# Kernel optimization log

Hardware: AMD Instinct MI355X
Metric: run time of the kernel (lower is better)

## Reference

```python
import jax, jax.numpy as jnp
import numpy as np

HIDDEN = 2048
INTER = 4096
NUM_EXPERTS = 8
TOP_K = 4
BATCH, SEQ = 2, 2048
TOKENS = BATCH * SEQ


def setup_inputs() -> dict:
    key = jax.random.key(0)
    k_x, k_rw, k_tw, k_te, k_gu, k_dn = jax.random.split(key, 6)
    x = jax.random.normal(k_x, (BATCH, SEQ, HIDDEN), dtype=jnp.float32)
    # full router weights (passed through but unused by this patched forward)
    weights = jax.random.uniform(k_rw, (TOKENS, NUM_EXPERTS), dtype=jnp.float32)
    tw = jax.random.uniform(k_tw, (TOKENS, TOP_K), dtype=jnp.float32)
    top_weights = tw / jnp.sum(tw, axis=-1, keepdims=True)  # softmax-like, renormalize=False downstream
    top_experts = jax.random.randint(k_te, (TOKENS, TOP_K), 0, NUM_EXPERTS, dtype=jnp.int64)
    scale_gu = 1.0 / np.sqrt(HIDDEN)
    scale_dn = 1.0 / np.sqrt(INTER)
    gate_up_weights = jax.random.normal(k_gu, (NUM_EXPERTS, 2 * INTER, HIDDEN), dtype=jnp.float32) * scale_gu
    down_weights = jax.random.normal(k_dn, (NUM_EXPERTS, HIDDEN, INTER), dtype=jnp.float32) * scale_dn
    return {
        'x': x,
        'weights': weights,
        'top_weights': top_weights,
        'top_experts': top_experts,
        'gate_up_weights': gate_up_weights,
        'down_weights': down_weights,
    }


def _fused_moe(xf, gate_up_weights, down_weights, top_weights, top_experts):
    """xf: [T, D]. Dense per-expert loop (scan over experts), masked combine.

    Matches fused_moe(renormalize=False): out[t] = sum_k top_weights[t,k] * expert_{top_experts[t,k]}(x[t])
    expert(x) = (silu(x @ Wg^T) * (x @ Wu^T)) @ Wd^T with [Wg; Wu] = gate_up.
    """
    E = gate_up_weights.shape[0]

    def step(out, inp):
        w_gu, w_d, e = inp
        # per-token combine coefficient for this expert (0 if not routed)
        coef = jnp.sum(jnp.where(top_experts == e, top_weights, 0.0), axis=-1)  # [T]
        h = xf @ w_gu.T                       # [T, 2*INTER]
        gate, up = jnp.split(h, 2, axis=-1)
        act = jax.nn.silu(gate) * up          # [T, INTER]
        o = act @ w_d.T                       # [T, D]
        return out + coef[:, None] * o, None

    out, _ = jax.lax.scan(step, jnp.zeros_like(xf),
                          (gate_up_weights, down_weights, jnp.arange(E, dtype=jnp.int64)))
    return out


def reference(x, weights, top_weights, top_experts, gate_up_weights, down_weights):
    B, S, D = x.shape
    xf = x.reshape(-1, D)  # flatten(0, 1)
    out = _fused_moe(xf, gate_up_weights, down_weights, top_weights, top_experts)
    return out.reshape(B, S, D)  # unflatten(0, (-1, q_len))
```

## Files before the change

### kernel.cpp

```cpp
#include <hip/hip_runtime.h>
#include <stdint.h>

#define T_TOKENS 4096
#define D_HID    2048
#define D_INT    4096
#define N_EXP    8
#define TOPK     4
#define NFLAT    (T_TOKENS*TOPK)
#define BM       128
#define MAXPAD   (NFLAT + N_EXP*BM)
#define MTILES   (MAXPAD/BM)

#define OFF_XB   0ull
#define OFF_ACT  16777216ull
#define OFF_PTOK 159383552ull
#define OFF_PWT  159453184ull
#define OFF_CNT  159522816ull
#define OFF_TOFF 159523072ull
#define OFF_SEG  159531264ull

typedef float f32x4  __attribute__((ext_vector_type(4)));
typedef short bf16x8 __attribute__((ext_vector_type(8)));

__device__ __forceinline__ unsigned short f2bf(float f) {
    unsigned int u = __float_as_uint(f);
    u += 0x7fffu + ((u >> 16) & 1u);
    return (unsigned short)(u >> 16);
}

__device__ __forceinline__ void gload_lds16(const void* g, void* l) {
    __builtin_amdgcn_global_load_lds((const __attribute__((address_space(1))) void*)g,
                                     (__attribute__((address_space(3))) void*)l,
                                     16, 0, 0);
}

__global__ void k_prep(const float* __restrict__ x, unsigned short* __restrict__ xb,
                       float* __restrict__ out) {
    int i = blockIdx.x * 256 + threadIdx.x;
    float4 v = ((const float4*)x)[i];
    ushort4 h;
    h.x = f2bf(v.x); h.y = f2bf(v.y); h.z = f2bf(v.z); h.w = f2bf(v.w);
    ((ushort4*)xb)[i] = h;
    ((float4*)out)[i] = make_float4(0.f, 0.f, 0.f, 0.f);
}

__global__ void k_count(const int* __restrict__ te, int* __restrict__ counts,
                        int* __restrict__ toff) {
    int e = blockIdx.x, t = threadIdx.x;
    int cnt = 0;
    int base = t * 64;
    for (int i = 0; i < 64; i++) cnt += (te[base + i] == e);
    __shared__ int s[256];
    s[t] = cnt; __syncthreads();
    int incl = cnt;
    for (int off = 1; off < 256; off <<= 1) {
        int tmp = (t >= off) ? s[t - off] : 0;
        __syncthreads();
        incl += tmp; s[t] = incl;
        __syncthreads();
    }
    toff[e * 256 + t] = incl - cnt;
    if (t == 255) counts[e] = incl;
}

__global__ void k_fill(const int* __restrict__ te, const float* __restrict__ tw,
                       const int* __restrict__ counts, const int* __restrict__ toff,
                       int* __restrict__ ptok, float* __restrict__ pwt, int* __restrict__ seg) {
    int e = blockIdx.x, t = threadIdx.x;
    int segs[9]; int a = 0;
    #pragma unroll
    for (int j = 0; j < 8; j++) { segs[j] = a; a += (counts[j] + BM - 1) & ~(BM - 1); }
    segs[8] = a;
    if (e == 0 && t == 0) { for (int j = 0; j < 9; j++) seg[j] = segs[j]; }
    int base = segs[e] + toff[e * 256 + t];
    int rank = 0;
    for (int i = t * 64; i < (t + 1) * 64; i++) {
        if (te[i] == e) { ptok[base + rank] = i >> 2; pwt[base + rank] = tw[i]; rank++; }
    }
    int cnt = counts[e], pc = (cnt + BM - 1) & ~(BM - 1);
    for (int i = cnt + t; i < pc; i += 256) { ptok[segs[e] + i] = -1; pwt[segs[e] + i] = 0.f; }
}

__launch_bounds__(256, 2)
__global__ void k_gemm1(const unsigned short* __restrict__ xb, const float* __restrict__ wgu,
                        const int* __restrict__ ptok, const int* __restrict__ seg,
                        unsigned short* __restrict__ act) {
    __shared__ char lds[32768];
    char* lA = lds; char* lB = lds + 16384;
    int nb = blockIdx.x, mb = blockIdx.y;
    if (mb * BM >= seg[8]) return;
    int e = 0;
    #pragma unroll
    for (int j = 1; j < 8; j++) if (seg[j] <= mb * BM) e = j;
    int tid = threadIdx.x, w = tid >> 6, l = tid & 63;

    const char* asrc[4]; char* adst[4];
    #pragma unroll
    for (int i = 0; i < 4; i++) {
        int row = w * 32 + i * 8 + (l >> 3);
        int tok = ptok[mb * BM + row]; if (tok < 0) tok = 0;
        int csrc = (l & 7) ^ (row & 7);
        asrc[i] = (const char*)(xb + (size_t)tok * D_HID + csrc * 8);
        adst[i] = lA + (w * 32 + i * 8) * 128;
    }
    const float* bsrc[8]; int bdst[8];
    #pragma unroll
    for (int j = 0; j < 8; j++) {
        int flat = j * 1024 + tid * 4;
        int r = flat >> 6, c = flat & 63;
        size_t grow = (r < 64) ? (size_t)(nb * 64 + r) : (size_t)(D_INT + nb * 64 + (r - 64));
        bsrc[j] = wgu + (size_t)e * 2 * D_INT * D_HID + grow * D_HID + c;
        bdst[j] = r * 128 + ((c * 2) ^ ((r & 7) << 4));
    }

    f32x4 acc[2][8];
    #pragma unroll
    for (int m = 0; m < 2; m++)
        #pragma unroll
        for (int n = 0; n < 8; n++) acc[m][n] = (f32x4){0.f, 0.f, 0.f, 0.f};

    for (int k0 = 0; k0 < D_HID; k0 += 64) {
        #pragma unroll
        for (int i = 0; i < 4; i++) gload_lds16(asrc[i] + (size_t)k0 * 2, adst[i]);
        #pragma unroll
        for (int j = 0; j < 8; j++) {
            float4 v = *(const float4*)(bsrc[j] + k0);
            ushort4 h;
            h.x = f2bf(v.x); h.y = f2bf(v.y); h.z = f2bf(v.z); h.w = f2bf(v.w);
            *(ushort4*)(lB + bdst[j]) = h;
        }
        __syncthreads();
        #pragma unroll
        for (int kk = 0; kk < 2; kk++) {
            bf16x8 a[2], b[8];
            #pragma unroll
            for (int m = 0; m < 2; m++) {
                int row = w * 32 + m * 16 + (l & 15);
                int kb = kk * 64 + (l >> 4) * 16;
                a[m] = *(const bf16x8*)(lA + row * 128 + (kb ^ ((row & 7) << 4)));
            }
            #pragma unroll
            for (int n = 0; n < 8; n++) {
                int row = n * 16 + (l & 15);
                int kb = kk * 64 + (l >> 4) * 16;
                b[n] = *(const bf16x8*)(lB + row * 128 + (kb ^ ((row & 7) << 4)));
            }
            #pragma unroll
            for (int m = 0; m < 2; m++)
                #pragma unroll
                for (int n = 0; n < 8; n++)
                    acc[m][n] = __builtin_amdgcn_mfma_f32_16x16x32_bf16(a[m], b[n], acc[m][n], 0, 0, 0);
        }
        __syncthreads();
    }
    #pragma unroll
    for (int m = 0; m < 2; m++)
        #pragma unroll
        for (int n = 0; n < 4; n++) {
            f32x4 g = acc[m][n], u = acc[m][n + 4];
            #pragma unroll
            for (int r = 0; r < 4; r++) {
                float gv = g[r], uv = u[r];
                float av = gv / (1.f + __expf(-gv)) * uv;
                int row = w * 32 + m * 16 + (l >> 4) * 4 + r;
                int col = nb * 64 + n * 16 + (l & 15);
                act[(size_t)(mb * BM + row) * D_INT + col] = f2bf(av);
            }
        }
}

__launch_bounds__(256, 2)
__global__ void k_gemm2(const unsigned short* __restrict__ act, const float* __restrict__ wd,
                        const int* __restrict__ ptok, const float* __restrict__ pwt,
                        const int* __restrict__ seg, float* __restrict__ out) {
    __shared__ char lds[32768];
    char* lA = lds; char* lB = lds + 16384;
    int nb = blockIdx.x, mb = blockIdx.y;
    if (mb * BM >= seg[8]) return;
    int e = 0;
    #pragma unroll
    for (int j = 1; j < 8; j++) if (seg[j] <= mb * BM) e = j;
    int tid = threadIdx.x, w = tid >> 6, l = tid & 63;

    const char* asrc[4]; char* adst[4];
    #pragma unroll
    for (int i = 0; i < 4; i++) {
        int row = w * 32 + i * 8 + (l >> 3);
        int csrc = (l & 7) ^ (row & 7);
        asrc[i] = (const char*)(act + (size_t)(mb * BM + row) * D_INT + csrc * 8);
        adst[i] = lA + (w * 32 + i * 8) * 128;
    }
    const float* bsrc[8]; int bdst[8];
    #pragma unroll
    for (int j = 0; j < 8; j++) {
        int flat = j * 1024 + tid * 4;
        int r = flat >> 6, c = flat & 63;
        bsrc[j] = wd + (size_t)e * D_HID * D_INT + (size_t)(nb * BM + r) * D_INT + c;
        bdst[j] = r * 128 + ((c * 2) ^ ((r & 7) << 4));
    }

    f32x4 acc[2][8];
    #pragma unroll
    for (int m = 0; m < 2; m++)
        #pragma unroll
        for (int n = 0; n < 8; n++) acc[m][n] = (f32x4){0.f, 0.f, 0.f, 0.f};

    for (int k0 = 0; k0 < D_INT; k0 += 64) {
        #pragma unroll
        for (int i = 0; i < 4; i++) gload_lds16(asrc[i] + (size_t)k0 * 2, adst[i]);
        #pragma unroll
        for (int j = 0; j < 8; j++) {
            float4 v = *(const float4*)(bsrc[j] + k0);
            ushort4 h;
            h.x = f2bf(v.x); h.y = f2bf(v.y); h.z = f2bf(v.z); h.w = f2bf(v.w);
            *(ushort4*)(lB + bdst[j]) = h;
        }
        __syncthreads();
        #pragma unroll
        for (int kk = 0; kk < 2; kk++) {
            bf16x8 a[2], b[8];
            #pragma unroll
            for (int m = 0; m < 2; m++) {
                int row = w * 32 + m * 16 + (l & 15);
                int kb = kk * 64 + (l >> 4) * 16;
                a[m] = *(const bf16x8*)(lA + row * 128 + (kb ^ ((row & 7) << 4)));
            }
            #pragma unroll
            for (int n = 0; n < 8; n++) {
                int row = n * 16 + (l & 15);
                int kb = kk * 64 + (l >> 4) * 16;
                b[n] = *(const bf16x8*)(lB + row * 128 + (kb ^ ((row & 7) << 4)));
            }
            #pragma unroll
            for (int m = 0; m < 2; m++)
                #pragma unroll
                for (int n = 0; n < 8; n++)
                    acc[m][n] = __builtin_amdgcn_mfma_f32_16x16x32_bf16(a[m], b[n], acc[m][n], 0, 0, 0);
        }
        __syncthreads();
    }
    #pragma unroll
    for (int m = 0; m < 2; m++) {
        #pragma unroll
        for (int r = 0; r < 4; r++) {
            int row = w * 32 + m * 16 + (l >> 4) * 4 + r;
            int p = mb * BM + row;
            int tok = ptok[p];
            float wt = pwt[p];
            if (tok >= 0) {
                #pragma unroll
                for (int n = 0; n < 8; n++) {
                    int col = nb * BM + n * 16 + (l & 15);
                    unsafeAtomicAdd(&out[(size_t)tok * D_HID + col], wt * acc[m][n][r]);
                }
            }
        }
    }
}

extern "C" void kernel_launch(void* const* d_in, const int* in_sizes, int n_in,
                              void* d_out, int out_size, void* d_ws, size_t ws_size,
                              hipStream_t stream) {
    const float* x   = (const float*)d_in[0];
    const float* tw  = (const float*)d_in[2];
    const int*   te  = (const int*)d_in[3];
    const float* wgu = (const float*)d_in[4];
    const float* wd  = (const float*)d_in[5];
    float* out = (float*)d_out;
    char*  ws  = (char*)d_ws;

    unsigned short* xb  = (unsigned short*)(ws + OFF_XB);
    unsigned short* act = (unsigned short*)(ws + OFF_ACT);
    int*   ptok   = (int*)(ws + OFF_PTOK);
    float* pwt    = (float*)(ws + OFF_PWT);
    int*   counts = (int*)(ws + OFF_CNT);
    int*   toff   = (int*)(ws + OFF_TOFF);
    int*   seg    = (int*)(ws + OFF_SEG);

    k_prep<<<8192, 256, 0, stream>>>(x, xb, out);
    k_count<<<N_EXP, 256, 0, stream>>>(te, counts, toff);
    k_fill<<<N_EXP, 256, 0, stream>>>(te, tw, counts, toff, ptok, pwt, seg);
    k_gemm1<<<dim3(D_INT / 64, MTILES), 256, 0, stream>>>(xb, wgu, ptok, seg, act);
    k_gemm2<<<dim3(D_HID / BM, MTILES), 256, 0, stream>>>(act, wd, ptok, pwt, seg, out);
}
```

Measured before the change: 1.378 ms.

## Pre-convert expert weights to bf16 once per call and remap blocks for XCD locality

Adds a conversion kernel that turns all gate_up and down weights into bf16 in the workspace, so the GEMM kernels can stream B tiles straight into LDS with global_load_lds instead of re-reading fp32 and converting per tile. This removes the repeated fp32 weight reads and conversions across the many M-tiles that share an expert. The cost is an extra full pass over the weights and a larger workspace; if the workspace is too small, the old fp32 path is used. The GEMM grids are also flattened and remapped so that consecutive M-tiles for the same N-tile land on the same XCD, which should improve L2 reuse of weights.

```diff
diff --git a/kernel.cpp b/kernel.cpp
--- a/kernel.cpp
+++ b/kernel.cpp
@@ -11,13 +11,16 @@
 #define MAXPAD   (NFLAT + N_EXP*BM)
 #define MTILES   (MAXPAD/BM)
 
-#define OFF_XB   0ull
-#define OFF_ACT  16777216ull
-#define OFF_PTOK 159383552ull
-#define OFF_PWT  159453184ull
-#define OFF_CNT  159522816ull
-#define OFF_TOFF 159523072ull
-#define OFF_SEG  159531264ull
+#define OFF_PTOK 0ull
+#define OFF_PWT  69632ull
+#define OFF_CNT  139264ull
+#define OFF_TOFF 139392ull
+#define OFF_SEG  147584ull
+#define OFF_XB   262144ull
+#define OFF_ACT  17039360ull
+#define OFF_WGU  159645696ull
+#define OFF_WD   428081152ull
+#define NEED_BF16 562298880ull
 
 typedef float f32x4  __attribute__((ext_vector_type(4)));
 typedef short bf16x8 __attribute__((ext_vector_type(8)));
@@ -32,6 +35,12 @@
     __builtin_amdgcn_global_load_lds((const __attribute__((address_space(1))) void*)g,
                                      (__attribute__((address_space(3))) void*)l,
                                      16, 0, 0);
+}
+
+__device__ __forceinline__ int xcd_logical(int hw, int nwg) {
+    int q = nwg >> 3, r = nwg & 7;
+    int xc = hw & 7, sl = hw >> 3;
+    return (xc < r ? xc * (q + 1) : r * (q + 1) + (xc - r) * q) + sl;
 }
 
 __global__ void k_prep(const float* __restrict__ x, unsigned short* __restrict__ xb,
@@ -42,6 +51,18 @@
     h.x = f2bf(v.x); h.y = f2bf(v.y); h.z = f2bf(v.z); h.w = f2bf(v.w);
     ((ushort4*)xb)[i] = h;
     ((float4*)out)[i] = make_float4(0.f, 0.f, 0.f, 0.f);
+}
+
+__global__ void k_conv(const float* __restrict__ wgu, const float* __restrict__ wd,
+                       unsigned short* __restrict__ wgu_b, unsigned short* __restrict__ wd_b) {
+    size_t i = (size_t)blockIdx.x * 256 + threadIdx.x;
+    const size_t NG4 = (size_t)N_EXP * 2 * D_INT * D_HID / 4;
+    float4 v; unsigned short* dst;
+    if (i < NG4) { v = ((const float4*)wgu)[i]; dst = wgu_b + i * 4; }
+    else { size_t j = i - NG4; v = ((const float4*)wd)[j]; dst = wd_b + j * 4; }
+    ushort4 h;
+    h.x = f2bf(v.x); h.y = f2bf(v.y); h.z = f2bf(v.z); h.w = f2bf(v.w);
+    *(ushort4*)dst = h;
 }
 
 __global__ void k_count(const int* __restrict__ te, int* __restrict__ counts,
@@ -81,13 +102,15 @@
     for (int i = cnt + t; i < pc; i += 256) { ptok[segs[e] + i] = -1; pwt[segs[e] + i] = 0.f; }
 }
 
+template<bool BF16W>
 __launch_bounds__(256, 2)
-__global__ void k_gemm1(const unsigned short* __restrict__ xb, const float* __restrict__ wgu,
+__global__ void k_gemm1(const unsigned short* __restrict__ xb, const void* __restrict__ wguv,
                         const int* __restrict__ ptok, const int* __restrict__ seg,
                         unsigned short* __restrict__ act) {
     __shared__ char lds[32768];
     char* lA = lds; char* lB = lds + 16384;
-    int nb = blockIdx.x, mb = blockIdx.y;
+    int logical = xcd_logical(blockIdx.x, gridDim.x);
+    int nb = logical / MTILES, mb = logical % MTILES;
     if (mb * BM >= seg[8]) return;
     int e = 0;
     #pragma unroll
@@ -103,14 +126,30 @@
         asrc[i] = (const char*)(xb + (size_t)tok * D_HID + csrc * 8);
         adst[i] = lA + (w * 32 + i * 8) * 128;
     }
-    const float* bsrc[8]; int bdst[8];
-    #pragma unroll
-    for (int j = 0; j < 8; j++) {
-        int flat = j * 1024 + tid * 4;
-        int r = flat >> 6, c = flat & 63;
-        size_t grow = (r < 64) ? (size_t)(nb * 64 + r) : (size_t)(D_INT + nb * 64 + (r - 64));
-        bsrc[j] = wgu + (size_t)e * 2 * D_INT * D_HID + grow * D_HID + c;
-        bdst[j] = r * 128 + ((c * 2) ^ ((r & 7) << 4));
+
+    const unsigned short* bsrc16[4]; char* bdst16[4];
+    const float* bsrc32[8]; int bdst32[8];
+    if constexpr (BF16W) {
+        const unsigned short* wb = (const unsigned short*)wguv + (size_t)e * 2 * D_INT * D_HID;
+        #pragma unroll
+        for (int i = 0; i < 4; i++) {
+            int rrow = w * 32 + i * 8 + (l >> 3);
+            size_t grow = (rrow < 64) ? (size_t)(nb * 64 + rrow)
+                                      : (size_t)(D_INT + nb * 64 + (rrow - 64));
+            int csrc = (l & 7) ^ (rrow & 7);
+            bsrc16[i] = wb + grow * D_HID + csrc * 8;
+            bdst16[i] = lB + (w * 32 + i * 8) * 128;
+        }
+    } else {
+        const float* wgu = (const float*)wguv;
+        #pragma unroll
+        for (int j = 0; j < 8; j++) {
+            int flat = j * 1024 + tid * 4;
+            int r = flat >> 6, c = flat & 63;
+            size_t grow = (r < 64) ? (size_t)(nb * 64 + r) : (size_t)(D_INT + nb * 64 + (r - 64));
+            bsrc32[j] = wgu + (size_t)e * 2 * D_INT * D_HID + grow * D_HID + c;
+            bdst32[j] = r * 128 + ((c * 2) ^ ((r & 7) << 4));
+        }
     }
 
     f32x4 acc[2][8];
@@ -122,12 +161,17 @@
     for (int k0 = 0; k0 < D_HID; k0 += 64) {
         #pragma unroll
         for (int i = 0; i < 4; i++) gload_lds16(asrc[i] + (size_t)k0 * 2, adst[i]);
-        #pragma unroll
-        for (int j = 0; j < 8; j++) {
-            float4 v = *(const float4*)(bsrc[j] + k0);
-            ushort4 h;
-            h.x = f2bf(v.x); h.y = f2bf(v.y); h.z = f2bf(v.z); h.w = f2bf(v.w);
-            *(ushort4*)(lB + bdst[j]) = h;
+        if constexpr (BF16W) {
+            #pragma unroll
+            for (int i = 0; i < 4; i++) gload_lds16(bsrc16[i] + k0, bdst16[i]);
+        } else {
+            #pragma unroll
+            for (int j = 0; j < 8; j++) {
+                float4 v = *(const float4*)(bsrc32[j] + k0);
+                ushort4 h;
+                h.x = f2bf(v.x); h.y = f2bf(v.y); h.z = f2bf(v.z); h.w = f2bf(v.w);
+                *(ushort4*)(lB + bdst32[j]) = h;
+            }
         }
         __syncthreads();
         #pragma unroll
@@ -169,13 +213,15 @@
         }
 }
 
+template<bool BF16W>
 __launch_bounds__(256, 2)
-__global__ void k_gemm2(const unsigned short* __restrict__ act, const float* __restrict__ wd,
+__global__ void k_gemm2(const unsigned short* __restrict__ act, const void* __restrict__ wdv,
                         const int* __restrict__ ptok, const float* __restrict__ pwt,
                         const int* __restrict__ seg, float* __restrict__ out) {
     __shared__ char lds[32768];
     char* lA = lds; char* lB = lds + 16384;
-    int nb = blockIdx.x, mb = blockIdx.y;
+    int logical = xcd_logical(blockIdx.x, gridDim.x);
+    int nb = logical / MTILES, mb = logical % MTILES;
     if (mb * BM >= seg[8]) return;
     int e = 0;
     #pragma unroll
@@ -190,13 +236,26 @@
         asrc[i] = (const char*)(act + (size_t)(mb * BM + row) * D_INT + csrc * 8);
         adst[i] = lA + (w * 32 + i * 8) * 128;
     }
-    const float* bsrc[8]; int bdst[8];
-    #pragma unroll
-    for (int j = 0; j < 8; j++) {
-        int flat = j * 1024 + tid * 4;
-        int r = flat >> 6, c = flat & 63;
-        bsrc[j] = wd + (size_t)e * D_HID * D_INT + (size_t)(nb * BM + r) * D_INT + c;
-        bdst[j] = r * 128 + ((c * 2) ^ ((r & 7) << 4));
+    const unsigned short* bsrc16[4]; char* bdst16[4];
+    const float* bsrc32[8]; int bdst32[8];
+    if constexpr (BF16W) {
+        const unsigned short* wb = (const unsigned short*)wdv + (size_t)e * D_HID * D_INT;
+        #pragma unroll
+        for (int i = 0; i < 4; i++) {
+            int rrow = w * 32 + i * 8 + (l >> 3);
+            int csrc = (l & 7) ^ (rrow & 7);
+            bsrc16[i] = wb + (size_t)(nb * BM + rrow) * D_INT + csrc * 8;
+            bdst16[i] = lB + (w * 32 + i * 8) * 128;
+        }
+    } else {
+        const float* wd = (const float*)wdv;
+        #pragma unroll
+        for (int j = 0; j < 8; j++) {
+            int flat = j * 1024 + tid * 4;
+            int r = flat >> 6, c = flat & 63;
+            bsrc32[j] = wd + (size_t)e * D_HID * D_INT + (size_t)(nb * BM + r) * D_INT + c;
+            bdst32[j] = r * 128 + ((c * 2) ^ ((r & 7) << 4));
+        }
     }
 
     f32x4 acc[2][8];
@@ -208,12 +267,17 @@
     for (int k0 = 0; k0 < D_INT; k0 += 64) {
         #pragma unroll
         for (int i = 0; i < 4; i++) gload_lds16(asrc[i] + (size_t)k0 * 2, adst[i]);
-        #pragma unroll
-        for (int j = 0; j < 8; j++) {
-            float4 v = *(const float4*)(bsrc[j] + k0);
-            ushort4 h;
-            h.x = f2bf(v.x); h.y = f2bf(v.y); h.z = f2bf(v.z); h.w = f2bf(v.w);
-            *(ushort4*)(lB + bdst[j]) = h;
+        if constexpr (BF16W) {
+            #pragma unroll
+            for (int i = 0; i < 4; i++) gload_lds16(bsrc16[i] + k0, bdst16[i]);
+        } else {
+            #pragma unroll
+            for (int j = 0; j < 8; j++) {
+                float4 v = *(const float4*)(bsrc32[j] + k0);
+                ushort4 h;
+                h.x = f2bf(v.x); h.y = f2bf(v.y); h.z = f2bf(v.z); h.w = f2bf(v.w);
+                *(ushort4*)(lB + bdst32[j]) = h;
+            }
         }
         __syncthreads();
         #pragma unroll
@@ -269,17 +333,26 @@
     float* out = (float*)d_out;
     char*  ws  = (char*)d_ws;
 
-    unsigned short* xb  = (unsigned short*)(ws + OFF_XB);
-    unsigned short* act = (unsigned short*)(ws + OFF_ACT);
     int*   ptok   = (int*)(ws + OFF_PTOK);
     float* pwt    = (float*)(ws + OFF_PWT);
     int*   counts = (int*)(ws + OFF_CNT);
     int*   toff   = (int*)(ws + OFF_TOFF);
     int*   seg    = (int*)(ws + OFF_SEG);
+    unsigned short* xb    = (unsigned short*)(ws + OFF_XB);
+    unsigned short* act   = (unsigned short*)(ws + OFF_ACT);
+    unsigned short* wgu_b = (unsigned short*)(ws + OFF_WGU);
+    unsigned short* wd_b  = (unsigned short*)(ws + OFF_WD);
 
     k_prep<<<8192, 256, 0, stream>>>(x, xb, out);
     k_count<<<N_EXP, 256, 0, stream>>>(te, counts, toff);
     k_fill<<<N_EXP, 256, 0, stream>>>(te, tw, counts, toff, ptok, pwt, seg);
-    k_gemm1<<<dim3(D_INT / 64, MTILES), 256, 0, stream>>>(xb, wgu, ptok, seg, act);
-    k_gemm2<<<dim3(D_HID / BM, MTILES), 256, 0, stream>>>(act, wd, ptok, pwt, seg, out);
-}
+
+    if (ws_size >= NEED_BF16) {
+        k_conv<<<196608, 256, 0, stream>>>(wgu, wd, wgu_b, wd_b);
+        k_gemm1<true><<<(D_INT / 64) * MTILES, 256, 0, stream>>>(xb, wgu_b, ptok, seg, act);
+        k_gemm2<true><<<(D_HID / BM) * MTILES, 256, 0, stream>>>(act, wd_b, ptok, pwt, seg, out);
+    } else {
+        k_gemm1<false><<<(D_INT / 64) * MTILES, 256, 0, stream>>>(xb, wgu, ptok, seg, act);
+        k_gemm2<false><<<(D_HID / BM) * MTILES, 256, 0, stream>>>(act, wd, ptok, pwt, seg, out);
+    }
+}
```

After: 1.209 ms. -12.3%, faster.
